# Optimization experiments

Hardware: AMD Instinct MI355X
Metric: run time of the kernel (lower is better)

Reference implementation:

```python
import jax, jax.numpy as jnp
import numpy as np
from jax import lax

DN = ('NCHW', 'OIHW', 'NCHW')


def _bilinear(img, py, px):
    # img: [B,C,H,W]; py,px: [B,K2,H,W] float sampling coords (zero outside)
    B, C, H, W = img.shape
    y0 = jnp.floor(py); x0 = jnp.floor(px)
    wy1 = py - y0; wy0 = 1.0 - wy1
    wx1 = px - x0; wx0 = 1.0 - wx1

    def gather(yi, xi):
        yc = jnp.clip(yi, 0, H - 1).astype(jnp.int32)
        xc = jnp.clip(xi, 0, W - 1).astype(jnp.int32)
        valid = ((yi >= 0) & (yi <= H - 1) & (xi >= 0) & (xi <= W - 1)).astype(img.dtype)
        # per-batch advanced gather -> [B,C,K2,H,W]
        g = jax.vmap(lambda im, a, b: im[:, a, b])(img, yc, xc)
        return g * valid[:, None]

    return (gather(y0, x0) * (wy0 * wx0)[:, None]
            + gather(y0, x0 + 1) * (wy0 * wx1)[:, None]
            + gather(y0 + 1, x0) * (wy1 * wx0)[:, None]
            + gather(y0 + 1, x0 + 1) * (wy1 * wx1)[:, None])


def _deform_layer(x, ow, ob, w, b, dil=1):
    # offset conv: 3x3, stride 1, pad 1 -> [B, 18, H, W]
    B, C, H, W = x.shape
    off = lax.conv_general_dilated(x, ow, (1, 1), 'SAME', dimension_numbers=DN)
    off = off + ob[None, :, None, None]
    off = off.reshape(B, 9, 2, H, W)  # per kernel point: (dy, dx)
    oy, ox = off[:, :, 0], off[:, :, 1]
    ky, kx = jnp.meshgrid(jnp.arange(3), jnp.arange(3), indexing='ij')
    ky = ky.reshape(9).astype(x.dtype); kx = kx.reshape(9).astype(x.dtype)
    yy = jnp.arange(H, dtype=x.dtype)[:, None]
    xx = jnp.arange(W, dtype=x.dtype)[None, :]
    # sampling coords: out_pos - pad + dil*k + offset (pad == dil)
    py = yy[None, None] - dil + dil * ky[None, :, None, None] + oy
    px = xx[None, None] - dil + dil * kx[None, :, None, None] + ox
    sam = _bilinear(x, py, px)  # [B,C,9,H,W]
    out = jnp.einsum('bckhw,ock->bohw', sam, w.reshape(w.shape[0], C, 9))
    return out + b[None, :, None, None]


def setup_inputs() -> dict:
    key = jax.random.key(0)
    ks = jax.random.split(key, 5)
    L, C = 4, 256
    x = jax.random.normal(ks[0], (2, C, 96, 96), dtype=jnp.float32)
    # small offset-conv weights -> moderate offsets (torch inits them to 0)
    off_w = jax.random.normal(ks[1], (L, 18, C, 3, 3), dtype=jnp.float32) * 0.01
    off_b = jnp.zeros((L, 18), dtype=jnp.float32)
    fan_in = C * 9
    dw = jax.random.normal(ks[2], (L, C, C, 3, 3), dtype=jnp.float32) * np.sqrt(2.0 / fan_in)
    db = jnp.zeros((L, C), dtype=jnp.float32)
    return {'x': x, 'off_w': off_w, 'off_b': off_b, 'dw': dw, 'db': db}


def reference(x, off_w, off_b, dw, db):
    L = off_w.shape[0]
    for i in range(L):
        x = _deform_layer(x, off_w[i], off_b[i], dw[i], db[i], dil=1)
        x = jax.nn.relu(x)
    return x
```

## Files before the change

kernel.cpp:

```cpp
#include <hip/hip_runtime.h>

#define BN 2
#define CH 256
#define HH 96
#define WW 96
#define NL 4
#define HW (HH*WW)
#define KK (CH*9)
#define NPOS (BN*HW)

#define MPOS 32
#define NBLK (NPOS/MPOS)
#define CKCH 32
#define CKLEN (CKCH*9)
#define NCKS 4
#define SAMW2 296

#define WB_PER_L (288*256*8)
#define WB_TOT (NL*WB_PER_L)
#define OWB_PER_L (288*32*8)
#define OWB_TOT (NL*OWB_PER_L)

typedef __attribute__((ext_vector_type(8))) short short8;
typedef __attribute__((ext_vector_type(4))) float f32x4;

__device__ __forceinline__ unsigned short f2bf(float f) {
    union { float f; unsigned int u; } v; v.f = f;
    unsigned int r = v.u + 0x7fffu + ((v.u >> 16) & 1u);
    return (unsigned short)(r >> 16);
}

__global__ void prep_kernel(const float* __restrict__ dw, const float* __restrict__ off_w,
                            unsigned short* __restrict__ wB, unsigned short* __restrict__ owB) {
    int idx = blockIdx.x * 256 + threadIdx.x;
    if (idx < WB_TOT) {
        int j  = idx & 7;
        int oc = (idx >> 3) & 255;
        int g  = (idx >> 11) % 288;
        int l  = idx / WB_PER_L;
        int col = g * 8 + j;
        int ck = col / CKLEN;
        int r  = col - ck * CKLEN;
        int t9 = r >> 5;
        int ci = r & 31;
        int c  = ck * CKCH + ci;
        wB[idx] = f2bf(dw[((size_t)(l * CH + oc) * CH + c) * 9 + t9]);
    } else {
        int i2 = idx - WB_TOT;
        if (i2 >= OWB_TOT) return;
        int j   = i2 & 7;
        int ocp = (i2 >> 3) & 31;
        int g   = (i2 >> 8) % 288;
        int l   = i2 / OWB_PER_L;
        int col = g * 8 + j;
        int ck = col / CKLEN;
        int r  = col - ck * CKLEN;
        int t9 = r >> 5;
        int ci = r & 31;
        int c  = ck * CKCH + ci;
        owB[i2] = (ocp < 18) ? f2bf(off_w[((size_t)(l * 18 + ocp) * CH + c) * 9 + t9]) : 0;
    }
}

__global__ void __launch_bounds__(256)
transpose_kernel(const float* __restrict__ src, unsigned short* __restrict__ xT) {
    __shared__ float tile[64][65];
    int blk = blockIdx.x;
    int b = blk / 576, r = blk - 576 * b;
    int hw0 = (r >> 2) * 64, c0 = (r & 3) * 64;
    int tid = threadIdx.x;
    int lane = tid & 63, grp = tid >> 6;
    const float* sp = src + (size_t)(b * CH + c0) * HW + hw0;
    #pragma unroll
    for (int i = 0; i < 16; ++i) {
        int c = grp * 16 + i;
        tile[c][lane] = sp[(size_t)c * HW + lane];
    }
    __syncthreads();
    unsigned short* dp = xT + (size_t)(b * HW + hw0) * CH + c0;
    #pragma unroll
    for (int i = 0; i < 16; ++i) {
        int hw = grp * 16 + i;
        dp[(size_t)hw * CH + lane] = f2bf(tile[lane][hw]);
    }
}

__global__ void __launch_bounds__(256)
off_mfma_kernel(const unsigned short* __restrict__ xT, const unsigned short* __restrict__ owB,
                const float* __restrict__ ob, float* __restrict__ off_g) {
    __shared__ __align__(16) unsigned short sam[MPOS * SAMW2];
    __shared__ int rtab[288 * 2];
    const int tid = threadIdx.x;
    int pb = (int)blockIdx.x;
    pb = (pb & 7) * (NBLK / 8) + (pb >> 3);
    const int pos0 = pb * MPOS;
    const int b0   = pos0 / HW;
    const int rem0 = pos0 - b0 * HW;
    const int h0   = rem0 / WW;
    const int w0   = rem0 - h0 * WW;

    for (int rec = tid; rec < 288; rec += 256) {
        int p = rec / 9, t9 = rec - 9 * p;
        int dy = t9 / 3 - 1, dx = t9 - 3 * (t9 / 3) - 1;
        int y = h0 + dy, xw = w0 + p + dx;
        bool valid = ((unsigned)y < HH) && ((unsigned)xw < WW);
        rtab[2 * rec]     = valid ? (y * WW + xw) * CH : -1;
        rtab[2 * rec + 1] = p * SAMW2 + t9 * 32;
    }

    const int m   = tid & 15;
    const int q   = (tid >> 4) & 3;
    const int wvi = tid >> 6;
    const int mt  = wvi & 1;
    const int nt  = wvi >> 1;
    f32x4 aoff = {};
    const unsigned short* xTb = xT + (size_t)b0 * HW * CH;

    for (int ck = 0; ck < 8; ++ck) {
        __syncthreads();
        #pragma unroll
        for (int i = 0; i < 18; ++i) {
            int slot = i * 256 + tid;
            int rec = slot >> 4, cp = slot & 15;
            int s0 = rtab[2 * rec];
            int d0 = rtab[2 * rec + 1];
            unsigned int v = 0;
            if (s0 >= 0) __builtin_memcpy(&v, xTb + s0 + ck * CKCH + cp * 2, 4);
            *(unsigned int*)(sam + d0 + cp * 2) = v;
        }
        __syncthreads();
        const unsigned short* arow = sam + (mt * 16 + m) * SAMW2 + q * 8;
        #pragma unroll
        for (int kb = 0; kb < 9; ++kb) {
            short8 av = *(const short8*)(arow + kb * 32);
            short8 bv = *(const short8*)(owB + ((size_t)((ck * 36 + kb * 4 + q) * 32)
                                                + nt * 16 + m) * 8);
            aoff = __builtin_amdgcn_mfma_f32_16x16x32_bf16(av, bv, aoff, 0, 0, 0);
        }
    }
    int oc = nt * 16 + m;
    if (oc < 18) {
        float bsv = ob[oc];
        #pragma unroll
        for (int r = 0; r < 4; ++r) {
            int p = mt * 16 + q * 4 + r;
            off_g[(size_t)(pos0 + p) * 18 + oc] = aoff[r] + bsv;
        }
    }
}

__global__ void __launch_bounds__(256, 5)
deform_mfma_kernel(const unsigned short* __restrict__ xT, const float* __restrict__ off_g,
                   const unsigned short* __restrict__ wB,
                   float* __restrict__ dst0, float* __restrict__ dst1) {
    __shared__ __align__(16) unsigned short sam[MPOS * SAMW2];
    __shared__ float offs[MPOS * 18];
    __shared__ __align__(16) uint4 taps4[MPOS * 9];
    __shared__ unsigned short dso16[MPOS * 9];
    const int tid = threadIdx.x;
    const int s   = (int)blockIdx.x & 1;
    int pb = (int)blockIdx.x >> 1;
    pb = (pb & 7) * (NBLK / 8) + (pb >> 3);
    const int pos0 = pb * MPOS;
    const int b0   = pos0 / HW;
    const int rem0 = pos0 - b0 * HW;
    const int h0   = rem0 / WW;
    const int w0   = rem0 - h0 * WW;

    for (int i = tid; i < MPOS * 18; i += 256)
        offs[i] = off_g[(size_t)pos0 * 18 + i];
    __syncthreads();

    for (int rec = tid; rec < MPOS * 9; rec += 256) {
        int p  = rec / 9, t9 = rec - 9 * p;
        int ky = t9 / 3, kx = t9 - 3 * (t9 / 3);
        float py = (float)(h0 - 1 + ky) + offs[p * 18 + 2 * t9];
        float px = (float)(w0 + p - 1 + kx) + offs[p * 18 + 2 * t9 + 1];
        float yf = floorf(py), xf = floorf(px);
        int y0 = (int)yf, x0 = (int)xf;
        float wy1 = py - yf, wx1 = px - xf;
        float fy0 = ((unsigned)y0       < HH) ? 1.f - wy1 : 0.f;
        float fy1 = ((unsigned)(y0 + 1) < HH) ? wy1       : 0.f;
        float fx0 = ((unsigned)x0       < WW) ? 1.f - wx1 : 0.f;
        float fx1 = ((unsigned)(x0 + 1) < WW) ? wx1       : 0.f;
        int y0c = min(max(y0, 0), HH - 1), y1c = min(max(y0 + 1, 0), HH - 1);
        int x0c = min(max(x0, 0), WW - 1), x1c = min(max(x0 + 1, 0), WW - 1);
        int bx  = min(max(x0, 0), WW - 2);
        float wA  = (x0c == bx     ? fx0 : 0.f) + (x1c == bx     ? fx1 : 0.f);
        float wBv = (x0c == bx + 1 ? fx0 : 0.f) + (x1c == bx + 1 ? fx1 : 0.f);
        uint4 tv;
        tv.x = (unsigned int)((y0c * WW + bx) * CH);
        tv.y = (unsigned int)((y1c * WW + bx) * CH);
        tv.z = (unsigned int)f2bf(fy0 * wA) | ((unsigned int)f2bf(fy0 * wBv) << 16);
        tv.w = (unsigned int)f2bf(fy1 * wA) | ((unsigned int)f2bf(fy1 * wBv) << 16);
        taps4[rec] = tv;
        dso16[rec] = (unsigned short)(p * SAMW2 + t9 * 32);
    }

    const int lane = tid & 63;
    const int wvi  = tid >> 6;
    const int cp   = lane & 15;
    const int rsub = lane >> 4;
    const int m    = tid & 15;
    const int q    = (tid >> 4) & 3;

    f32x4 acc[2][4] = {};
    const unsigned short* xTb = xT + (size_t)b0 * HW * CH;

    for (int ckl = 0; ckl < NCKS; ++ckl) {
        const int ck = s * NCKS + ckl;
        __syncthreads();
        const unsigned short* xs = xTb + ck * CKCH + cp * 2;
        #pragma unroll 3
        for (int rr = 0; rr < 18; ++rr) {
            int rec = wvi * 72 + rr * 4 + rsub;
            uint4 tv = taps4[rec];
            int dso  = dso16[rec];
            float u0 = __uint_as_float(tv.z << 16);
            float u1 = __uint_as_float(tv.z & 0xFFFF0000u);
            float u2 = __uint_as_float(tv.w << 16);
            float u3 = __uint_as_float(tv.w & 0xFFFF0000u);
            unsigned int A0, A1, C0, C1;
            __builtin_memcpy(&A0, xs + tv.x, 4);
            __builtin_memcpy(&A1, xs + tv.x + CH, 4);
            __builtin_memcpy(&C0, xs + tv.y, 4);
            __builtin_memcpy(&C1, xs + tv.y + CH, 4);
            float vl = __uint_as_float(A0 << 16) * u0
                     + __uint_as_float(A1 << 16) * u1
                     + __uint_as_float(C0 << 16) * u2
                     + __uint_as_float(C1 << 16) * u3;
            float vh = __uint_as_float(A0 & 0xFFFF0000u) * u0
                     + __uint_as_float(A1 & 0xFFFF0000u) * u1
                     + __uint_as_float(C0 & 0xFFFF0000u) * u2
                     + __uint_as_float(C1 & 0xFFFF0000u) * u3;
            unsigned int packed = (unsigned int)f2bf(vl) | ((unsigned int)f2bf(vh) << 16);
            *(unsigned int*)(sam + dso + cp * 2) = packed;
        }
        __syncthreads();
        const unsigned short* arow0 = sam + m * SAMW2 + q * 8;
        const unsigned short* arow1 = arow0 + 16 * SAMW2;
        const int g0 = ck * 36;
        for (int kb = 0; kb < 9; ++kb) {
            short8 av0 = *(const short8*)(arow0 + kb * 32);
            short8 av1 = *(const short8*)(arow1 + kb * 32);
            const unsigned short* wkb = wB + ((size_t)(g0 + kb * 4 + q) * 256
                                             + (wvi * 64 + m)) * 8;
            #pragma unroll
            for (int t = 0; t < 4; ++t) {
                short8 bv = *(const short8*)(wkb + t * 16 * 8);
                acc[0][t] = __builtin_amdgcn_mfma_f32_16x16x32_bf16(av0, bv, acc[0][t], 0, 0, 0);
                acc[1][t] = __builtin_amdgcn_mfma_f32_16x16x32_bf16(av1, bv, acc[1][t], 0, 0, 0);
            }
        }
    }

    float* dst = s ? dst1 : dst0;
    float* cT = (float*)sam;
    #pragma unroll
    for (int mt = 0; mt < 2; ++mt) {
        __syncthreads();
        #pragma unroll
        for (int t = 0; t < 4; ++t) {
            int oc = wvi * 64 + t * 16 + m;
            #pragma unroll
            for (int r = 0; r < 4; ++r)
                cT[oc * 17 + q * 4 + r] = acc[mt][t][r];
        }
        __syncthreads();
        float* dp = dst + (size_t)(pos0 + mt * 16) * CH + tid;
        #pragma unroll 4
        for (int p = 0; p < 16; ++p)
            dp[(size_t)p * CH] = cT[tid * 17 + p];
    }
}

__global__ void __launch_bounds__(256)
sum_cl_kernel(const float* __restrict__ p0, const float* __restrict__ p1,
              const float* __restrict__ db, unsigned short* __restrict__ xT) {
    unsigned int idx = blockIdx.x * 256 + threadIdx.x;
    unsigned int e = idx * 4;
    unsigned int oc = e & (CH - 1);
    float4 bsv = *(const float4*)(db + oc);
    float4 a = *(const float4*)(p0 + e);
    float4 b = *(const float4*)(p1 + e);
    unsigned short o[4];
    o[0] = f2bf(fmaxf(a.x + b.x + bsv.x, 0.f));
    o[1] = f2bf(fmaxf(a.y + b.y + bsv.y, 0.f));
    o[2] = f2bf(fmaxf(a.z + b.z + bsv.z, 0.f));
    o[3] = f2bf(fmaxf(a.w + b.w + bsv.w, 0.f));
    __builtin_memcpy(xT + e, o, 8);
}

__global__ void __launch_bounds__(256)
sum_nchw_kernel(const float* __restrict__ p0, const float* __restrict__ p1,
                const float* __restrict__ db, float* __restrict__ out) {
    __shared__ float tile[64][65];
    int blk = blockIdx.x;
    int hw0 = (blk >> 2) * 64;
    int oc0 = (blk & 3) * 64;
    int tid = threadIdx.x;
    int lane = tid & 63, grp = tid >> 6;
    float bsv = db[oc0 + lane];
    #pragma unroll
    for (int i = 0; i < 16; ++i) {
        int r = grp * 16 + i;
        size_t e = (size_t)(hw0 + r) * CH + oc0 + lane;
        tile[r][lane] = fmaxf(p0[e] + p1[e] + bsv, 0.f);
    }
    __syncthreads();
    int b = hw0 / HW, hwl = hw0 - b * HW;
    #pragma unroll
    for (int i = 0; i < 16; ++i) {
        int oc = grp * 16 + i;
        out[((size_t)(b * CH) + oc0 + oc) * HW + hwl + lane] = tile[lane][oc];
    }
}

extern "C" void kernel_launch(void* const* d_in, const int* in_sizes, int n_in,
                              void* d_out, int out_size, void* d_ws, size_t ws_size,
                              hipStream_t stream) {
    const float* x     = (const float*)d_in[0];
    const float* off_w = (const float*)d_in[1];
    const float* off_b = (const float*)d_in[2];
    const float* dw    = (const float*)d_in[3];
    const float* db    = (const float*)d_in[4];

    float* ws   = (float*)d_ws;
    float* p0    = ws;
    float* p1    = p0 + (size_t)NPOS * CH;
    float* off_g = p1 + (size_t)NPOS * CH;
    unsigned short* wB  = (unsigned short*)(off_g + (size_t)NPOS * 18);
    unsigned short* owB = wB + WB_TOT;
    unsigned short* xT  = owB + OWB_TOT;

    prep_kernel<<<(WB_TOT + OWB_TOT + 255) / 256, 256, 0, stream>>>(dw, off_w, wB, owB);
    transpose_kernel<<<BN * 576, 256, 0, stream>>>(x, xT);

    for (int l = 0; l < NL; ++l) {
        off_mfma_kernel<<<NBLK, 256, 0, stream>>>(
            xT, owB + (size_t)l * OWB_PER_L, off_b + l * 18, off_g);
        deform_mfma_kernel<<<NBLK * 2, 256, 0, stream>>>(
            xT, off_g, wB + (size_t)l * WB_PER_L, p0, p1);
        if (l < NL - 1)
            sum_cl_kernel<<<(NPOS * CH / 4) / 256, 256, 0, stream>>>(p0, p1, db + l * CH, xT);
        else
            sum_nchw_kernel<<<(NPOS / 64) * 4, 256, 0, stream>>>(p0, p1, db + l * CH,
                                                                 (float*)d_out);
    }
}
```

Before: 493.3 us.

## Load offset-conv MFMA operands directly from global and pair FMAs in bilinear sampling

The offset convolution kernel no longer stages an im2col tile in shared memory with per-chunk barriers. Each lane now loads its short8 A operand straight from the transposed activations using a precomputed tap table, and two accumulators alternate to break the MFMA dependency chain. The deform kernel's bilinear blend is rewritten as paired fmaf chains, which may help the compiler emit packed FMAs. The trade-off is more uncoalesced global loads, redundant across waves, in exchange for dropping the LDS traffic and synchronisation.

Result: faster. 434.7 us (-11.9%).

```diff
diff --git a/kernel.cpp b/kernel.cpp
--- a/kernel.cpp
+++ b/kernel.cpp
@@ -88,8 +88,7 @@
 __global__ void __launch_bounds__(256)
 off_mfma_kernel(const unsigned short* __restrict__ xT, const unsigned short* __restrict__ owB,
                 const float* __restrict__ ob, float* __restrict__ off_g) {
-    __shared__ __align__(16) unsigned short sam[MPOS * SAMW2];
-    __shared__ int rtab[288 * 2];
+    __shared__ int rtab[MPOS * 9];
     const int tid = threadIdx.x;
     int pb = (int)blockIdx.x;
     pb = (pb & 7) * (NBLK / 8) + (pb >> 3);
@@ -99,43 +98,36 @@
     const int h0   = rem0 / WW;
     const int w0   = rem0 - h0 * WW;
 
-    for (int rec = tid; rec < 288; rec += 256) {
+    for (int rec = tid; rec < MPOS * 9; rec += 256) {
         int p = rec / 9, t9 = rec - 9 * p;
         int dy = t9 / 3 - 1, dx = t9 - 3 * (t9 / 3) - 1;
         int y = h0 + dy, xw = w0 + p + dx;
         bool valid = ((unsigned)y < HH) && ((unsigned)xw < WW);
-        rtab[2 * rec]     = valid ? (y * WW + xw) * CH : -1;
-        rtab[2 * rec + 1] = p * SAMW2 + t9 * 32;
-    }
+        rtab[rec] = valid ? (y * WW + xw) * CH : -1;
+    }
+    __syncthreads();
 
     const int m   = tid & 15;
     const int q   = (tid >> 4) & 3;
     const int wvi = tid >> 6;
     const int mt  = wvi & 1;
     const int nt  = wvi >> 1;
-    f32x4 aoff = {};
-    const unsigned short* xTb = xT + (size_t)b0 * HW * CH;
-
-    for (int ck = 0; ck < 8; ++ck) {
-        __syncthreads();
+    const int p   = mt * 16 + m;
+
+    const unsigned short* xq = xT + (size_t)b0 * HW * CH + q * 8;
+    const unsigned short* wq = owB + (size_t)(nt * 16 + m) * 8;
+
+    f32x4 acc0 = {}, acc1 = {};
+    for (int kb = 0; kb < 9; ++kb) {
+        int s0 = rtab[p * 9 + kb];
+        const unsigned short* ap = xq + s0;
         #pragma unroll
-        for (int i = 0; i < 18; ++i) {
-            int slot = i * 256 + tid;
-            int rec = slot >> 4, cp = slot & 15;
-            int s0 = rtab[2 * rec];
-            int d0 = rtab[2 * rec + 1];
-            unsigned int v = 0;
-            if (s0 >= 0) __builtin_memcpy(&v, xTb + s0 + ck * CKCH + cp * 2, 4);
-            *(unsigned int*)(sam + d0 + cp * 2) = v;
-        }
-        __syncthreads();
-        const unsigned short* arow = sam + (mt * 16 + m) * SAMW2 + q * 8;
-        #pragma unroll
-        for (int kb = 0; kb < 9; ++kb) {
-            short8 av = *(const short8*)(arow + kb * 32);
-            short8 bv = *(const short8*)(owB + ((size_t)((ck * 36 + kb * 4 + q) * 32)
-                                                + nt * 16 + m) * 8);
-            aoff = __builtin_amdgcn_mfma_f32_16x16x32_bf16(av, bv, aoff, 0, 0, 0);
+        for (int ck = 0; ck < 8; ++ck) {
+            short8 av = {};
+            if (s0 >= 0) av = *(const short8*)(ap + ck * CKCH);
+            short8 bv = *(const short8*)(wq + (size_t)(ck * 36 + kb * 4 + q) * (32 * 8));
+            if (ck & 1) acc1 = __builtin_amdgcn_mfma_f32_16x16x32_bf16(av, bv, acc1, 0, 0, 0);
+            else        acc0 = __builtin_amdgcn_mfma_f32_16x16x32_bf16(av, bv, acc0, 0, 0, 0);
         }
     }
     int oc = nt * 16 + m;
@@ -143,8 +135,8 @@
         float bsv = ob[oc];
         #pragma unroll
         for (int r = 0; r < 4; ++r) {
-            int p = mt * 16 + q * 4 + r;
-            off_g[(size_t)(pos0 + p) * 18 + oc] = aoff[r] + bsv;
+            int pp = mt * 16 + q * 4 + r;
+            off_g[(size_t)(pos0 + pp) * 18 + oc] = acc0[r] + acc1[r] + bsv;
         }
     }
 }
@@ -225,15 +217,16 @@
             __builtin_memcpy(&A1, xs + tv.x + CH, 4);
             __builtin_memcpy(&C0, xs + tv.y, 4);
             __builtin_memcpy(&C1, xs + tv.y + CH, 4);
-            float vl = __uint_as_float(A0 << 16) * u0
-                     + __uint_as_float(A1 << 16) * u1
-                     + __uint_as_float(C0 << 16) * u2
-                     + __uint_as_float(C1 << 16) * u3;
-            float vh = __uint_as_float(A0 & 0xFFFF0000u) * u0
-                     + __uint_as_float(A1 & 0xFFFF0000u) * u1
-                     + __uint_as_float(C0 & 0xFFFF0000u) * u2
-                     + __uint_as_float(C1 & 0xFFFF0000u) * u3;
-            unsigned int packed = (unsigned int)f2bf(vl) | ((unsigned int)f2bf(vh) << 16);
+            float2 a0 = make_float2(__uint_as_float(A0 << 16), __uint_as_float(A0 & 0xFFFF0000u));
+            float2 a1 = make_float2(__uint_as_float(A1 << 16), __uint_as_float(A1 & 0xFFFF0000u));
+            float2 c0 = make_float2(__uint_as_float(C0 << 16), __uint_as_float(C0 & 0xFFFF0000u));
+            float2 c1 = make_float2(__uint_as_float(C1 << 16), __uint_as_float(C1 & 0xFFFF0000u));
+            float2 vv;
+            vv.x = a0.x * u0;               vv.y = a0.y * u0;
+            vv.x = fmaf(a1.x, u1, vv.x);    vv.y = fmaf(a1.y, u1, vv.y);
+            vv.x = fmaf(c0.x, u2, vv.x);    vv.y = fmaf(c0.y, u2, vv.y);
+            vv.x = fmaf(c1.x, u3, vv.x);    vv.y = fmaf(c1.y, u3, vv.y);
+            unsigned int packed = (unsigned int)f2bf(vv.x) | ((unsigned int)f2bf(vv.y) << 16);
             *(unsigned int*)(sam + dso + cp * 2) = packed;
         }
         __syncthreads();
```
